# Performance work log

Hardware: AMD Instinct MI355X
Metric: run time of the kernel (lower is better)

The kernel has to match this reference:

```python
import jax, jax.numpy as jnp
import numpy as np

HIDDEN = 768
NUM_BLOCKS = 8
BLOCK = HIDDEN // NUM_BLOCKS
LAMBDA = 0.01
SCALE = 0.02


def softshrink(v, lam):
    return jnp.sign(v) * jnp.maximum(jnp.abs(v) - lam, 0.0)


def setup_inputs() -> dict:
    key = jax.random.key(0)
    ks = jax.random.split(key, 5)
    B, S = 4, 8192
    x = jax.random.normal(ks[0], (B, S, HIDDEN), dtype=jnp.float32)
    w1 = SCALE * jax.random.normal(ks[1], (2, NUM_BLOCKS, BLOCK, BLOCK), dtype=jnp.float32)
    b1 = SCALE * jax.random.normal(ks[2], (2, NUM_BLOCKS, BLOCK), dtype=jnp.float32)
    w2 = SCALE * jax.random.normal(ks[3], (2, NUM_BLOCKS, BLOCK, BLOCK), dtype=jnp.float32)
    b2 = SCALE * jax.random.normal(ks[4], (2, NUM_BLOCKS, BLOCK), dtype=jnp.float32)
    return {"x": x, "w1": w1, "b1": b1, "w2": w2, "b2": b2}


def reference(x, w1, b1, w2, b2):
    bias = x
    dtype = x.dtype
    xf = x.astype(jnp.float32)
    B, S, C = xf.shape
    M = S // 2 + 1  # total modes; hard_thresholding_fraction=1.0 -> all kept
    X = jnp.fft.rfft(xf, axis=1, norm="ortho")  # [B, M, C] complex64
    X = X.reshape(B, M, NUM_BLOCKS, BLOCK)
    xr, xi = X.real, X.imag
    # layer 1: complex block-diagonal matmul + relu
    mul = lambda inp, w: jnp.einsum("bmnd,ndk->bmnk", inp, w)
    o1r = jax.nn.relu(mul(xr, w1[0]) - mul(xi, w1[1]) + b1[0])
    o1i = jax.nn.relu(mul(xi, w1[0]) + mul(xr, w1[1]) + b1[1])
    # layer 2
    o2r = mul(o1r, w2[0]) - mul(o1i, w2[1]) + b2[0]
    o2i = mul(o1r, w2[1]) + mul(o1i, w2[0]) + b2[1]
    # softshrink applied elementwise to real and imag parts
    o2r = softshrink(o2r, LAMBDA)
    o2i = softshrink(o2i, LAMBDA)
    Y = (o2r + 1j * o2i).reshape(B, M, C)
    y = jnp.fft.irfft(Y, n=S, axis=1, norm="ortho").astype(dtype)
    return y + bias
```

## Files before the change

### kernel.cpp

```cpp
#include <hip/hip_runtime.h>
#include <hip/hip_bf16.h>

#define HIDDEN 768
#define NB 8
#define BLK 96
#define S_LEN 8192
#define H_LEN 4096
#define M_LEN 4097
#define MP 4160
#define BATCH 4
#define KBIG 192
#define TMOD 64
#define APITCH 100

#define TWO_PI 6.28318530717958647692f
#define INV_SQRT_N 0.011048543456039806f
#define C_INV 0.022097086912079612f
#define LAM 0.01f

typedef __attribute__((ext_vector_type(8))) short short8;
typedef __attribute__((ext_vector_type(4))) float float4v;

__device__ __forceinline__ short f2bf(float f) {
    __hip_bfloat16 h = __float2bfloat16(f);
    return *reinterpret_cast<short*>(&h);
}
__device__ __forceinline__ float bf2f(unsigned short s) {
    __hip_bfloat16 h = *reinterpret_cast<__hip_bfloat16*>(&s);
    return __bfloat162float(h);
}
__device__ __forceinline__ float2 cmul(float2 a, float2 b) {
    return make_float2(a.x * b.x - a.y * b.y, a.x * b.y + a.y * b.x);
}

__global__ __launch_bounds__(256) void prep_weights(const float* __restrict__ w1,
                                                    const float* __restrict__ w2,
                                                    const float* __restrict__ b1,
                                                    const float* __restrict__ b2,
                                                    short* __restrict__ WT1,
                                                    short* __restrict__ WT2,
                                                    float* __restrict__ bb1,
                                                    float* __restrict__ bb2) {
    int idx = blockIdx.x * 256 + threadIdx.x;
    if (idx < NB * KBIG * KBIG) {
        int n = idx / (KBIG * KBIG);
        int r = idx % (KBIG * KBIG);
        int o = r / KBIG;
        int kin = r % KBIG;
        int d = kin >> 1;
        int im = kin & 1;
        {
            float w0 = w1[((size_t)(0 * NB + n) * BLK + d) * BLK + (o < BLK ? o : o - BLK)];
            float wi = w1[((size_t)(1 * NB + n) * BLK + d) * BLK + (o < BLK ? o : o - BLK)];
            float v = (o < BLK) ? (im ? -wi : w0) : (im ? w0 : wi);
            WT1[idx] = f2bf(v);
        }
        {
            float w0 = w2[((size_t)(0 * NB + n) * BLK + d) * BLK + (o < BLK ? o : o - BLK)];
            float wi = w2[((size_t)(1 * NB + n) * BLK + d) * BLK + (o < BLK ? o : o - BLK)];
            float v = (o < BLK) ? (im ? -wi : w0) : (im ? w0 : wi);
            WT2[idx] = f2bf(v);
        }
    }
    if (idx < NB * KBIG) {
        int n = idx / KBIG, o = idx % KBIG;
        bb1[idx] = (o < BLK) ? b1[(0 * NB + n) * BLK + o] : b1[(1 * NB + n) * BLK + o - BLK];
        bb2[idx] = (o < BLK) ? b2[(0 * NB + n) * BLK + o] : b2[(1 * NB + n) * BLK + o - BLK];
    }
}

__global__ __launch_bounds__(256) void init_twiddles(float2* __restrict__ tw4k,
                                                     float2* __restrict__ tw8k) {
    int i = blockIdx.x * 256 + threadIdx.x;
    if (i < 4096) {
        float ang = -TWO_PI * (float)i * (1.0f / 4096.0f);
        tw4k[i] = make_float2(cosf(ang), sinf(ang));
    }
    if (i <= 4096) {
        float ang = -TWO_PI * (float)i * (1.0f / 8192.0f);
        tw8k[i] = make_float2(cosf(ang), sinf(ang));
    }
}

__global__ __launch_bounds__(256) void transpose_in(const float* __restrict__ x,
                                                    __hip_bfloat16* __restrict__ xT) {
    __shared__ float t[32][33];
    const int cb = blockIdx.x, sb = blockIdx.y, b = blockIdx.z;
    const int tx = threadIdx.x & 31, ty = threadIdx.x >> 5;
    const float* xp = x + ((size_t)b * S_LEN + sb * 32) * HIDDEN + cb * 32;
    for (int i = 0; i < 4; i++)
        t[ty + 8 * i][tx] = xp[(size_t)(ty + 8 * i) * HIDDEN + tx];
    __syncthreads();
    __hip_bfloat16* xq = xT + ((size_t)b * HIDDEN + cb * 32) * S_LEN + sb * 32;
    for (int i = 0; i < 4; i++)
        xq[(size_t)(ty + 8 * i) * S_LEN + tx] = __float2bfloat16(t[tx][ty + 8 * i]);
}

template<bool INV>
__device__ __forceinline__ void dft16(float2* v) {
    const float s3 = INV ? -1.f : 1.f;
    constexpr float C1 = 0.92387953251128674f;
    constexpr float S1 = 0.38268343236508977f;
    constexpr float R2 = 0.70710678118654752f;
    float2 a[16];
    #pragma unroll
    for (int na = 0; na < 4; na++) {
        float2 x0 = v[na], x1 = v[na + 4], x2 = v[na + 8], x3 = v[na + 12];
        float t0x = x0.x + x2.x, t0y = x0.y + x2.y;
        float t1x = x0.x - x2.x, t1y = x0.y - x2.y;
        float t2x = x1.x + x3.x, t2y = x1.y + x3.y;
        float t3x = x1.x - x3.x, t3y = x1.y - x3.y;
        a[na]      = make_float2(t0x + t2x, t0y + t2y);
        a[na + 8]  = make_float2(t0x - t2x, t0y - t2y);
        a[na + 4]  = make_float2(t1x + s3 * t3y, t1y - s3 * t3x);
        a[na + 12] = make_float2(t1x - s3 * t3y, t1y + s3 * t3x);
    }
    auto tw = [s3](float2 z, float ce, float se) {
        return make_float2(z.x * ce + s3 * z.y * se, z.y * ce - s3 * z.x * se);
    };
    a[5]  = tw(a[5],  C1,  S1);
    a[6]  = tw(a[6],  R2,  R2);
    a[7]  = tw(a[7],  S1,  C1);
    a[9]  = tw(a[9],  R2,  R2);
    a[10] = tw(a[10], 0.f, 1.f);
    a[11] = tw(a[11], -R2, R2);
    a[13] = tw(a[13], S1,  C1);
    a[14] = tw(a[14], -R2, R2);
    a[15] = tw(a[15], -C1, -S1);
    #pragma unroll
    for (int kb = 0; kb < 4; kb++) {
        float2 x0 = a[4 * kb], x1 = a[4 * kb + 1], x2 = a[4 * kb + 2], x3 = a[4 * kb + 3];
        float t0x = x0.x + x2.x, t0y = x0.y + x2.y;
        float t1x = x0.x - x2.x, t1y = x0.y - x2.y;
        float t2x = x1.x + x3.x, t2y = x1.y + x3.y;
        float t3x = x1.x - x3.x, t3y = x1.y - x3.y;
        v[kb]      = make_float2(t0x + t2x, t0y + t2y);
        v[kb + 8]  = make_float2(t0x - t2x, t0y - t2y);
        v[kb + 4]  = make_float2(t1x + s3 * t3y, t1y - s3 * t3x);
        v[kb + 12] = make_float2(t1x - s3 * t3y, t1y + s3 * t3x);
    }
}

template<bool INV>
__device__ __forceinline__ void fft3pass(float2* v, float2* arr,
                                         const float2* __restrict__ tw4k, int t) {
    const float sg = INV ? -1.f : 1.f;
    const int n0 = t & 15;
    const int hi = t >> 4;

    dft16<INV>(v);
    arr[n0 * 17 + hi] = v[0];
    #pragma unroll
    for (int p = 1; p < 16; p++) {
        float2 w = tw4k[(t * p) & 4095];
        arr[(n0 + 16 * p) * 17 + hi] = cmul(v[p], make_float2(w.x, sg * w.y));
    }
    __syncthreads();

    #pragma unroll
    for (int n1 = 0; n1 < 16; n1++) v[n1] = arr[t * 17 + n1];
    __syncthreads();
    dft16<INV>(v);
    arr[hi * 17 + n0] = v[0];
    #pragma unroll
    for (int q = 1; q < 16; q++) {
        float2 w = tw4k[(16 * n0 * q) & 4095];
        arr[(hi + 16 * q) * 17 + n0] = cmul(v[q], make_float2(w.x, sg * w.y));
    }
    __syncthreads();

    #pragma unroll
    for (int i = 0; i < 16; i++) v[i] = arr[t * 17 + i];
    dft16<INV>(v);
}

__global__ __launch_bounds__(256, 4) void fft_fwd(const __hip_bfloat16* __restrict__ xT,
                                                  unsigned int* __restrict__ Xc,
                                                  const float2* __restrict__ tw4k,
                                                  const float2* __restrict__ tw8k) {
    __shared__ float2 arr[256 * 17];
    const int wg = blockIdx.x;
    const int t = threadIdx.x;
    const __hip_bfloat162* xrow = (const __hip_bfloat162*)(xT + (size_t)wg * S_LEN);

    float2 v[16];
    #pragma unroll
    for (int j = 0; j < 16; j++) {
        __hip_bfloat162 pz = xrow[t + 256 * j];
        v[j] = make_float2(__bfloat162float(pz.x), __bfloat162float(pz.y));
    }

    fft3pass<false>(v, arr, tw4k, t);

    __syncthreads();
    #pragma unroll
    for (int k0 = 0; k0 < 16; k0++) arr[t + 256 * k0] = v[k0];
    __syncthreads();

    unsigned int* Xrow = Xc + (size_t)wg * MP;
    for (int m = t; m <= H_LEN; m += 256) {
        int ia = m & (H_LEN - 1);
        int ib = (H_LEN - m) & (H_LEN - 1);
        float2 za = arr[ia];
        float2 zb = arr[ib];
        float er = 0.5f * (za.x + zb.x), ei = 0.5f * (za.y - zb.y);
        float dr = za.x - zb.x, di = za.y + zb.y;
        float or_ = 0.5f * di, oi = -0.5f * dr;
        float2 tt = tw8k[m];
        float xrv = (er + tt.x * or_ - tt.y * oi) * INV_SQRT_N;
        float xiv = (ei + tt.x * oi + tt.y * or_) * INV_SQRT_N;
        unsigned wd = (unsigned short)f2bf(xrv) | ((unsigned)(unsigned short)f2bf(xiv) << 16);
        Xrow[m] = wd;
    }
}

__global__ __launch_bounds__(256) void mlp_mfma(const short* __restrict__ WT1,
                                                const short* __restrict__ WT2,
                                                const float* __restrict__ bb1,
                                                const float* __restrict__ bb2,
                                                unsigned int* __restrict__ Xc) {
    __shared__ unsigned int actA[TMOD * APITCH];
    __shared__ unsigned int actB[TMOD * APITCH];
    const int tid = threadIdx.x;
    const int chunk = blockIdx.x;
    const int n = blockIdx.y;
    const int b = blockIdx.z;
    const int m0 = chunk * TMOD;
    unsigned int* __restrict__ Xrow0 =
        Xc + ((size_t)b * HIDDEN + (size_t)n * BLK) * MP + m0;

    {
        const int mw = tid & 31;
        const int dr = tid >> 5;
        for (int pass = 0; pass < 12; pass++) {
            int d = dr + pass * 8;
            uint2 v = ((const uint2*)(Xrow0 + (size_t)d * MP))[mw];
            actA[(2 * mw) * APITCH + d] = v.x;
            actA[(2 * mw + 1) * APITCH + d] = v.y;
        }
    }

    const int w = tid >> 6;
    const int l15 = tid & 15;
    const int q = (tid >> 4) & 3;
    const int outw = w * 48;

    short8 wf[3][6], wf2[3][6];
    for (int nl = 0; nl < 3; nl++)
        for (int ks = 0; ks < 6; ks++) {
            wf[nl][ks]  = *(const short8*)(WT1 + ((size_t)n * KBIG + outw + nl * 16 + l15) * KBIG + ks * 32 + q * 8);
            wf2[nl][ks] = *(const short8*)(WT2 + ((size_t)n * KBIG + outw + nl * 16 + l15) * KBIG + ks * 32 + q * 8);
        }

    __syncthreads();

    for (int mt = 0; mt < 4; mt++) {
        float4v acc[3];
        for (int nl = 0; nl < 3; nl++)
            acc[nl] = *(const float4v*)(bb1 + n * KBIG + outw + nl * 16 + q * 4);
        #pragma unroll
        for (int ks = 0; ks < 6; ks++) {
            short8 bf = *(const short8*)(&actA[(mt * 16 + l15) * APITCH + ks * 16 + q * 4]);
            acc[0] = __builtin_amdgcn_mfma_f32_16x16x32_bf16(wf[0][ks], bf, acc[0], 0, 0, 0);
            acc[1] = __builtin_amdgcn_mfma_f32_16x16x32_bf16(wf[1][ks], bf, acc[1], 0, 0, 0);
            acc[2] = __builtin_amdgcn_mfma_f32_16x16x32_bf16(wf[2][ks], bf, acc[2], 0, 0, 0);
        }
        short* sb = (short*)actB;
        for (int nl = 0; nl < 3; nl++)
            #pragma unroll
            for (int reg = 0; reg < 4; reg++) {
                int o = outw + nl * 16 + q * 4 + reg;
                int si = (o < BLK) ? (o << 1) : (((o - BLK) << 1) | 1);
                sb[(mt * 16 + l15) * (2 * APITCH) + si] = f2bf(fmaxf(acc[nl][reg], 0.f));
            }
    }
    __syncthreads();

    for (int mt = 0; mt < 4; mt++) {
        float4v acc[3];
        for (int nl = 0; nl < 3; nl++)
            acc[nl] = *(const float4v*)(bb2 + n * KBIG + outw + nl * 16 + q * 4);
        #pragma unroll
        for (int ks = 0; ks < 6; ks++) {
            short8 bf = *(const short8*)(&actB[(mt * 16 + l15) * APITCH + ks * 16 + q * 4]);
            acc[0] = __builtin_amdgcn_mfma_f32_16x16x32_bf16(wf2[0][ks], bf, acc[0], 0, 0, 0);
            acc[1] = __builtin_amdgcn_mfma_f32_16x16x32_bf16(wf2[1][ks], bf, acc[1], 0, 0, 0);
            acc[2] = __builtin_amdgcn_mfma_f32_16x16x32_bf16(wf2[2][ks], bf, acc[2], 0, 0, 0);
        }
        short* sa = (short*)actA;
        for (int nl = 0; nl < 3; nl++)
            #pragma unroll
            for (int reg = 0; reg < 4; reg++) {
                int o = outw + nl * 16 + q * 4 + reg;
                float v = acc[nl][reg];
                v = copysignf(fmaxf(fabsf(v) - LAM, 0.f), v);
                int si = (o < BLK) ? (o << 1) : (((o - BLK) << 1) | 1);
                sa[(mt * 16 + l15) * (2 * APITCH) + si] = f2bf(v);
            }
    }
    __syncthreads();

    {
        const int mw = tid & 31;
        const int dr = tid >> 5;
        for (int pass = 0; pass < 12; pass++) {
            int d = dr + pass * 8;
            uint2 v;
            v.x = actA[(2 * mw) * APITCH + d];
            v.y = actA[(2 * mw + 1) * APITCH + d];
            ((uint2*)(Xrow0 + (size_t)d * MP))[mw] = v;
        }
    }
}

__global__ __launch_bounds__(256, 4) void fft_inv(const unsigned int* __restrict__ Xc,
                                                  __hip_bfloat16* __restrict__ yT,
                                                  const float2* __restrict__ tw4k,
                                                  const float2* __restrict__ tw8k) {
    __shared__ float2 arr[256 * 17];
    const int wg = blockIdx.x;
    const int t = threadIdx.x;
    const unsigned int* Xrow = Xc + (size_t)wg * MP;

    float2 v[16];
    #pragma unroll
    for (int j = 0; j < 16; j++) {
        int m = t + 256 * j;
        unsigned va = Xrow[m];
        unsigned vb = Xrow[H_LEN - m];
        float arv = bf2f((unsigned short)(va & 0xFFFF));
        float aiv = bf2f((unsigned short)(va >> 16));
        float brv = bf2f((unsigned short)(vb & 0xFFFF));
        float biv = bf2f((unsigned short)(vb >> 16));
        if (m == 0) { aiv = 0.f; biv = 0.f; }
        float er = 0.5f * (arv + brv), ei = 0.5f * (aiv - biv);
        float dr = arv - brv, di = aiv + biv;
        float2 tt = tw8k[m];
        float wcs = tt.x, wsn = -tt.y;
        float or_ = 0.5f * (wcs * dr - wsn * di);
        float oi = 0.5f * (wcs * di + wsn * dr);
        v[j] = make_float2(er - oi, ei + or_);
    }

    fft3pass<true>(v, arr, tw4k, t);

    __hip_bfloat162* orow = (__hip_bfloat162*)(yT + (size_t)wg * S_LEN);
    #pragma unroll
    for (int k0 = 0; k0 < 16; k0++) {
        __hip_bfloat162 w;
        w.x = __float2bfloat16(C_INV * v[k0].x);
        w.y = __float2bfloat16(C_INV * v[k0].y);
        orow[t + 256 * k0] = w;
    }
}

__global__ __launch_bounds__(256) void add_out(const __hip_bfloat16* __restrict__ yT,
                                               const float* __restrict__ x,
                                               float* __restrict__ out) {
    __shared__ float t[32][33];
    const int cb = blockIdx.x, sb = blockIdx.y, b = blockIdx.z;
    const int tx = threadIdx.x & 31, ty = threadIdx.x >> 5;
    const __hip_bfloat16* yp = yT + ((size_t)b * HIDDEN + cb * 32) * S_LEN + sb * 32;
    for (int i = 0; i < 4; i++)
        t[ty + 8 * i][tx] = __bfloat162float(yp[(size_t)(ty + 8 * i) * S_LEN + tx]);
    __syncthreads();
    const size_t off = ((size_t)b * S_LEN + sb * 32) * HIDDEN + cb * 32;
    const float* xp = x + off;
    float* op = out + off;
    for (int i = 0; i < 4; i++)
        op[(size_t)(ty + 8 * i) * HIDDEN + tx] =
            xp[(size_t)(ty + 8 * i) * HIDDEN + tx] + t[tx][ty + 8 * i];
}

extern "C" void kernel_launch(void* const* d_in, const int* in_sizes, int n_in,
                              void* d_out, int out_size, void* d_ws, size_t ws_size,
                              hipStream_t stream) {
    const float* x  = (const float*)d_in[0];
    const float* w1 = (const float*)d_in[1];
    const float* b1 = (const float*)d_in[2];
    const float* w2 = (const float*)d_in[3];
    const float* b2 = (const float*)d_in[4];
    float* out = (float*)d_out;

    char* p = (char*)d_ws;
    __hip_bfloat16* xT = (__hip_bfloat16*)p;           p += (size_t)BATCH * HIDDEN * S_LEN * 2;
    unsigned int*   Xc = (unsigned int*)p;             p += (size_t)BATCH * HIDDEN * MP * 4;
    short* WT1 = (short*)p;                            p += (size_t)NB * KBIG * KBIG * 2;
    short* WT2 = (short*)p;                            p += (size_t)NB * KBIG * KBIG * 2;
    float* bb1 = (float*)p;                            p += (size_t)NB * KBIG * 4;
    float* bb2 = (float*)p;                            p += (size_t)NB * KBIG * 4;
    float2* tw4k = (float2*)p;                         p += (size_t)4096 * sizeof(float2);
    float2* tw8k = (float2*)p;                         p += (size_t)4100 * sizeof(float2);

    prep_weights<<<(NB * KBIG * KBIG + 255) / 256, 256, 0, stream>>>(
        w1, w2, b1, b2, WT1, WT2, bb1, bb2);

    init_twiddles<<<17, 256, 0, stream>>>(tw4k, tw8k);

    transpose_in<<<dim3(HIDDEN / 32, S_LEN / 32, BATCH), 256, 0, stream>>>(x, xT);

    fft_fwd<<<BATCH * HIDDEN, 256, 0, stream>>>(xT, Xc, tw4k, tw8k);

    mlp_mfma<<<dim3(65, NB, BATCH), 256, 0, stream>>>(WT1, WT2, bb1, bb2, Xc);

    fft_inv<<<BATCH * HIDDEN, 256, 0, stream>>>(Xc, xT , tw4k, tw8k);

    add_out<<<dim3(HIDDEN / 32, S_LEN / 32, BATCH), 256, 0, stream>>>(xT, x, out);
}
```

Measured before the change: 396.0 us.

## Interleave real/imag weight rows and vectorize MLP LDS staging and stores

Reorders the packed weight and bias rows so real and imaginary outputs are interleaved. MFMA results can then be packed as bf16 pairs and written to LDS with one 8-byte store instead of scattered 2-byte stores. Global-to-LDS staging is rewritten to do 16-byte LDS stores per thread, and the layer-2 weight loads are deferred until after layer 1 to reduce register pressure, with a minimum-occupancy hint of 3 waves. Global accesses per instruction become 4-byte coalesced loads and stores instead of 8-byte ones.

```diff
diff --git a/kernel.cpp b/kernel.cpp
--- a/kernel.cpp
+++ b/kernel.cpp
@@ -28,6 +28,9 @@
 __device__ __forceinline__ float bf2f(unsigned short s) {
     __hip_bfloat16 h = *reinterpret_cast<__hip_bfloat16*>(&s);
     return __bfloat162float(h);
+}
+__device__ __forceinline__ unsigned pack2bf(float a, float b) {
+    return (unsigned)(unsigned short)f2bf(a) | ((unsigned)(unsigned short)f2bf(b) << 16);
 }
 __device__ __forceinline__ float2 cmul(float2 a, float2 b) {
     return make_float2(a.x * b.x - a.y * b.y, a.x * b.y + a.y * b.x);
@@ -45,27 +48,30 @@
     if (idx < NB * KBIG * KBIG) {
         int n = idx / (KBIG * KBIG);
         int r = idx % (KBIG * KBIG);
-        int o = r / KBIG;
+        int op = r / KBIG;
         int kin = r % KBIG;
+        int oc = op >> 1;
+        int oim = op & 1;
         int d = kin >> 1;
         int im = kin & 1;
         {
-            float w0 = w1[((size_t)(0 * NB + n) * BLK + d) * BLK + (o < BLK ? o : o - BLK)];
-            float wi = w1[((size_t)(1 * NB + n) * BLK + d) * BLK + (o < BLK ? o : o - BLK)];
-            float v = (o < BLK) ? (im ? -wi : w0) : (im ? w0 : wi);
+            float w0 = w1[((size_t)(0 * NB + n) * BLK + d) * BLK + oc];
+            float wi = w1[((size_t)(1 * NB + n) * BLK + d) * BLK + oc];
+            float v = oim ? (im ? w0 : wi) : (im ? -wi : w0);
             WT1[idx] = f2bf(v);
         }
         {
-            float w0 = w2[((size_t)(0 * NB + n) * BLK + d) * BLK + (o < BLK ? o : o - BLK)];
-            float wi = w2[((size_t)(1 * NB + n) * BLK + d) * BLK + (o < BLK ? o : o - BLK)];
-            float v = (o < BLK) ? (im ? -wi : w0) : (im ? w0 : wi);
+            float w0 = w2[((size_t)(0 * NB + n) * BLK + d) * BLK + oc];
+            float wi = w2[((size_t)(1 * NB + n) * BLK + d) * BLK + oc];
+            float v = oim ? (im ? w0 : wi) : (im ? -wi : w0);
             WT2[idx] = f2bf(v);
         }
     }
     if (idx < NB * KBIG) {
-        int n = idx / KBIG, o = idx % KBIG;
-        bb1[idx] = (o < BLK) ? b1[(0 * NB + n) * BLK + o] : b1[(1 * NB + n) * BLK + o - BLK];
-        bb2[idx] = (o < BLK) ? b2[(0 * NB + n) * BLK + o] : b2[(1 * NB + n) * BLK + o - BLK];
+        int n = idx / KBIG, op = idx % KBIG;
+        int oc = op >> 1, oim = op & 1;
+        bb1[idx] = oim ? b1[(1 * NB + n) * BLK + oc] : b1[(0 * NB + n) * BLK + oc];
+        bb2[idx] = oim ? b2[(1 * NB + n) * BLK + oc] : b2[(0 * NB + n) * BLK + oc];
     }
 }
 
@@ -178,7 +184,7 @@
                                                   unsigned int* __restrict__ Xc,
                                                   const float2* __restrict__ tw4k,
                                                   const float2* __restrict__ tw8k) {
-    __shared__ float2 arr[256 * 17];
+    __shared__ __align__(16) float2 arr[256 * 17];
     const int wg = blockIdx.x;
     const int t = threadIdx.x;
     const __hip_bfloat162* xrow = (const __hip_bfloat162*)(xT + (size_t)wg * S_LEN);
@@ -214,13 +220,13 @@
     }
 }
 
-__global__ __launch_bounds__(256) void mlp_mfma(const short* __restrict__ WT1,
-                                                const short* __restrict__ WT2,
-                                                const float* __restrict__ bb1,
-                                                const float* __restrict__ bb2,
-                                                unsigned int* __restrict__ Xc) {
-    __shared__ unsigned int actA[TMOD * APITCH];
-    __shared__ unsigned int actB[TMOD * APITCH];
+__global__ __launch_bounds__(256, 3) void mlp_mfma(const short* __restrict__ WT1,
+                                                   const short* __restrict__ WT2,
+                                                   const float* __restrict__ bb1,
+                                                   const float* __restrict__ bb2,
+                                                   unsigned int* __restrict__ Xc) {
+    __shared__ __align__(16) unsigned int actA[TMOD * APITCH];
+    __shared__ __align__(16) unsigned int actB[TMOD * APITCH];
     const int tid = threadIdx.x;
     const int chunk = blockIdx.x;
     const int n = blockIdx.y;
@@ -229,28 +235,27 @@
     unsigned int* __restrict__ Xrow0 =
         Xc + ((size_t)b * HIDDEN + (size_t)n * BLK) * MP + m0;
 
-    {
-        const int mw = tid & 31;
-        const int dr = tid >> 5;
-        for (int pass = 0; pass < 12; pass++) {
-            int d = dr + pass * 8;
-            uint2 v = ((const uint2*)(Xrow0 + (size_t)d * MP))[mw];
-            actA[(2 * mw) * APITCH + d] = v.x;
-            actA[(2 * mw + 1) * APITCH + d] = v.y;
-        }
-    }
-
     const int w = tid >> 6;
     const int l15 = tid & 15;
     const int q = (tid >> 4) & 3;
     const int outw = w * 48;
-
-    short8 wf[3][6], wf2[3][6];
+    const int mstg = tid & 63;
+
+    #pragma unroll
+    for (int dp = 0; dp < 6; dp++) {
+        int d0 = dp * 16 + w * 4;
+        uint4 vv;
+        vv.x = Xrow0[(size_t)(d0 + 0) * MP + mstg];
+        vv.y = Xrow0[(size_t)(d0 + 1) * MP + mstg];
+        vv.z = Xrow0[(size_t)(d0 + 2) * MP + mstg];
+        vv.w = Xrow0[(size_t)(d0 + 3) * MP + mstg];
+        *(uint4*)&actA[mstg * APITCH + d0] = vv;
+    }
+
+    short8 wf[3][6];
     for (int nl = 0; nl < 3; nl++)
-        for (int ks = 0; ks < 6; ks++) {
-            wf[nl][ks]  = *(const short8*)(WT1 + ((size_t)n * KBIG + outw + nl * 16 + l15) * KBIG + ks * 32 + q * 8);
-            wf2[nl][ks] = *(const short8*)(WT2 + ((size_t)n * KBIG + outw + nl * 16 + l15) * KBIG + ks * 32 + q * 8);
-        }
+        for (int ks = 0; ks < 6; ks++)
+            wf[nl][ks] = *(const short8*)(WT1 + ((size_t)n * KBIG + outw + nl * 16 + l15) * KBIG + ks * 32 + q * 8);
 
     __syncthreads();
 
@@ -265,15 +270,20 @@
             acc[1] = __builtin_amdgcn_mfma_f32_16x16x32_bf16(wf[1][ks], bf, acc[1], 0, 0, 0);
             acc[2] = __builtin_amdgcn_mfma_f32_16x16x32_bf16(wf[2][ks], bf, acc[2], 0, 0, 0);
         }
-        short* sb = (short*)actB;
-        for (int nl = 0; nl < 3; nl++)
-            #pragma unroll
-            for (int reg = 0; reg < 4; reg++) {
-                int o = outw + nl * 16 + q * 4 + reg;
-                int si = (o < BLK) ? (o << 1) : (((o - BLK) << 1) | 1);
-                sb[(mt * 16 + l15) * (2 * APITCH) + si] = f2bf(fmaxf(acc[nl][reg], 0.f));
-            }
-    }
+        #pragma unroll
+        for (int nl = 0; nl < 3; nl++) {
+            uint2 st;
+            st.x = pack2bf(fmaxf(acc[nl][0], 0.f), fmaxf(acc[nl][1], 0.f));
+            st.y = pack2bf(fmaxf(acc[nl][2], 0.f), fmaxf(acc[nl][3], 0.f));
+            *(uint2*)&actB[(mt * 16 + l15) * APITCH + outw / 2 + nl * 8 + q * 2] = st;
+        }
+    }
+
+    short8 wf2[3][6];
+    for (int nl = 0; nl < 3; nl++)
+        for (int ks = 0; ks < 6; ks++)
+            wf2[nl][ks] = *(const short8*)(WT2 + ((size_t)n * KBIG + outw + nl * 16 + l15) * KBIG + ks * 32 + q * 8);
+
     __syncthreads();
 
     for (int mt = 0; mt < 4; mt++) {
@@ -287,29 +297,29 @@
             acc[1] = __builtin_amdgcn_mfma_f32_16x16x32_bf16(wf2[1][ks], bf, acc[1], 0, 0, 0);
             acc[2] = __builtin_amdgcn_mfma_f32_16x16x32_bf16(wf2[2][ks], bf, acc[2], 0, 0, 0);
         }
-        short* sa = (short*)actA;
-        for (int nl = 0; nl < 3; nl++)
-            #pragma unroll
-            for (int reg = 0; reg < 4; reg++) {
-                int o = outw + nl * 16 + q * 4 + reg;
-                float v = acc[nl][reg];
-                v = copysignf(fmaxf(fabsf(v) - LAM, 0.f), v);
-                int si = (o < BLK) ? (o << 1) : (((o - BLK) << 1) | 1);
-                sa[(mt * 16 + l15) * (2 * APITCH) + si] = f2bf(v);
-            }
-    }
-    __syncthreads();
-
-    {
-        const int mw = tid & 31;
-        const int dr = tid >> 5;
-        for (int pass = 0; pass < 12; pass++) {
-            int d = dr + pass * 8;
-            uint2 v;
-            v.x = actA[(2 * mw) * APITCH + d];
-            v.y = actA[(2 * mw + 1) * APITCH + d];
-            ((uint2*)(Xrow0 + (size_t)d * MP))[mw] = v;
-        }
+        #pragma unroll
+        for (int nl = 0; nl < 3; nl++) {
+            float v0 = acc[nl][0], v1 = acc[nl][1], v2 = acc[nl][2], v3 = acc[nl][3];
+            v0 = copysignf(fmaxf(fabsf(v0) - LAM, 0.f), v0);
+            v1 = copysignf(fmaxf(fabsf(v1) - LAM, 0.f), v1);
+            v2 = copysignf(fmaxf(fabsf(v2) - LAM, 0.f), v2);
+            v3 = copysignf(fmaxf(fabsf(v3) - LAM, 0.f), v3);
+            uint2 st;
+            st.x = pack2bf(v0, v1);
+            st.y = pack2bf(v2, v3);
+            *(uint2*)&actA[(mt * 16 + l15) * APITCH + outw / 2 + nl * 8 + q * 2] = st;
+        }
+    }
+    __syncthreads();
+
+    #pragma unroll
+    for (int dp = 0; dp < 6; dp++) {
+        int d0 = dp * 16 + w * 4;
+        uint4 vv = *(const uint4*)&actA[mstg * APITCH + d0];
+        Xrow0[(size_t)(d0 + 0) * MP + mstg] = vv.x;
+        Xrow0[(size_t)(d0 + 1) * MP + mstg] = vv.y;
+        Xrow0[(size_t)(d0 + 2) * MP + mstg] = vv.z;
+        Xrow0[(size_t)(d0 + 3) * MP + mstg] = vv.w;
     }
 }
 
@@ -317,7 +327,7 @@
                                                   __hip_bfloat16* __restrict__ yT,
                                                   const float2* __restrict__ tw4k,
                                                   const float2* __restrict__ tw8k) {
-    __shared__ float2 arr[256 * 17];
+    __shared__ __align__(16) float2 arr[256 * 17];
     const int wg = blockIdx.x;
     const int t = threadIdx.x;
     const unsigned int* Xrow = Xc + (size_t)wg * MP;
```

After: 387.7 us. 2.1% less time.
